# Kernel optimization log

Hardware: AMD Instinct MI355X
Metric: run time of the kernel (lower is better)

Reference implementation:

```python
import jax, jax.numpy as jnp
import numpy as np

TARGET_H, TARGET_W = 352, 352
# source spatial sizes for bottom1..bottom11 (all exact divisors of 352)
SRC_SIZES = [176, 88, 44, 22, 11, 176, 88, 44, 22, 11, 176]


def _block_resize(x, H, W):
    """Faithful jax version of simple_resize: nearest-neighbor block upsample
    with integer-floor steps, zero-filled remainder (zero here since sizes divide)."""
    h, w = x.shape[2], x.shape[3]
    xs, ys = H // h, W // w
    r = jnp.repeat(jnp.repeat(x, xs, axis=2), ys, axis=3)  # (1,1,h*xs,w*ys)
    return jnp.pad(r, ((0, 0), (0, 0), (0, H - r.shape[2]), (0, W - r.shape[3])))


def setup_inputs() -> dict:
    key = jax.random.key(0)
    keys = jax.random.split(key, 12)
    inp = {"bottom0": jax.random.normal(keys[0], (1, 1, TARGET_H, TARGET_W), dtype=jnp.float32)}
    for i, s in enumerate(SRC_SIZES, start=1):
        inp[f"bottom{i}"] = jax.random.normal(keys[i], (1, 1, s, s), dtype=jnp.float32)
    return inp


def reference(bottom0, bottom1, bottom2, bottom3, bottom4, bottom5,
              bottom6, bottom7, bottom8, bottom9, bottom10, bottom11):
    H, W = bottom0.shape[2], bottom0.shape[3]
    rest = [bottom1, bottom2, bottom3, bottom4, bottom5, bottom6,
            bottom7, bottom8, bottom9, bottom10, bottom11]
    datum = [bottom0]
    for b in rest:
        datum.append(b if b.shape == bottom0.shape else _block_resize(b, H, W))
    return jnp.concatenate(datum, axis=1)  # (1, 12, 352, 352)
```

## Files before the change

### kernel.cpp

```cpp
#include <hip/hip_runtime.h>


#define TARGET 352
#define PLANE (TARGET * TARGET)

struct Ptrs { const float* p[12]; };

__global__ __launch_bounds__(256) void resize_cat_kernel(Ptrs ptrs, float* __restrict__ out) {
    const int c = blockIdx.y;
    const int t = blockIdx.x * blockDim.x + threadIdx.x;
    const int e = t * 4;
    const int y = e / TARGET;
    const int x = e - y * TARGET;

    static const __device__ int d_shift[12] = {0, 1, 2, 3, 4, 5, 1, 2, 3, 4, 5, 1};
    static const __device__ int d_srcsz[12] = {TARGET, 176, 88, 44, 22, 11, 176, 88, 44, 22, 11, 176};

    const int sh = d_shift[c];
    const int s  = d_srcsz[c];
    const float* __restrict__ src = ptrs.p[c];

    float4 v;
    if (sh == 0) {
        v = *reinterpret_cast<const float4*>(src + e);
    } else {
        const float* row = src + (y >> sh) * s;
        if (sh >= 2) {
            const float vv = row[x >> sh];
            v = make_float4(vv, vv, vv, vv);
        } else {
            const float a = row[x >> 1];
            const float b = row[(x >> 1) + 1];
            v = make_float4(a, a, b, b);
        }
    }
    *reinterpret_cast<float4*>(out + c * PLANE + e) = v;
}

extern "C" void kernel_launch(void* const* d_in, const int* in_sizes, int n_in,
                              void* d_out, int out_size, void* d_ws, size_t ws_size,
                              hipStream_t stream) {
    Ptrs ptrs;
    for (int i = 0; i < 12; ++i) ptrs.p[i] = (const float*)d_in[i];
    float* out = (float*)d_out;

    dim3 grid(121, 12);
    resize_cat_kernel<<<grid, 256, 0, stream>>>(ptrs, out);
}
```

Baseline: 11.18 us.

## Process four channels per thread with compile-time resize parameters

Each thread now produces four output channels instead of one, and the grid shrinks from 12 to 3 channel groups. Shift and source size become template constants, so the device-memory lookup tables and runtime branching go away. The intent is more memory operations in flight per thread and less per-thread index overhead. In exchange, the grid has only 363 blocks, which may underfill the GPU's compute units and reduce the latency hiding that many blocks provide.

```diff
diff --git a/kernel.cpp b/kernel.cpp
--- a/kernel.cpp
+++ b/kernel.cpp
@@ -6,35 +6,53 @@
 
 struct Ptrs { const float* p[12]; };
 
+template <int SH, int SRCSZ>
+__device__ __forceinline__ float4 fetch(const float* __restrict__ src, int e, int y, int x) {
+    if constexpr (SH == 0) {
+        return *reinterpret_cast<const float4*>(src + e);
+    } else if constexpr (SH == 1) {
+        const float* row = src + (y >> 1) * SRCSZ;
+        const float a = row[x >> 1];
+        const float b = row[(x >> 1) + 1];
+        return make_float4(a, a, b, b);
+    } else {
+        const float* row = src + (y >> SH) * SRCSZ;
+        const float v = row[x >> SH];
+        return make_float4(v, v, v, v);
+    }
+}
+
+
 __global__ __launch_bounds__(256) void resize_cat_kernel(Ptrs ptrs, float* __restrict__ out) {
-    const int c = blockIdx.y;
+    const int g = blockIdx.y;
     const int t = blockIdx.x * blockDim.x + threadIdx.x;
     const int e = t * 4;
     const int y = e / TARGET;
     const int x = e - y * TARGET;
 
-    static const __device__ int d_shift[12] = {0, 1, 2, 3, 4, 5, 1, 2, 3, 4, 5, 1};
-    static const __device__ int d_srcsz[12] = {TARGET, 176, 88, 44, 22, 11, 176, 88, 44, 22, 11, 176};
+    float4 v0, v1, v2, v3;
+    if (g == 0) {
+        v0 = fetch<0, TARGET>(ptrs.p[0], e, y, x);
+        v1 = fetch<1, 176  >(ptrs.p[1], e, y, x);
+        v2 = fetch<2, 88   >(ptrs.p[2], e, y, x);
+        v3 = fetch<3, 44   >(ptrs.p[3], e, y, x);
+    } else if (g == 1) {
+        v0 = fetch<4, 22   >(ptrs.p[4], e, y, x);
+        v1 = fetch<5, 11   >(ptrs.p[5], e, y, x);
+        v2 = fetch<1, 176  >(ptrs.p[6], e, y, x);
+        v3 = fetch<2, 88   >(ptrs.p[7], e, y, x);
+    } else {
+        v0 = fetch<3, 44   >(ptrs.p[8], e, y, x);
+        v1 = fetch<4, 22   >(ptrs.p[9], e, y, x);
+        v2 = fetch<5, 11   >(ptrs.p[10], e, y, x);
+        v3 = fetch<1, 176  >(ptrs.p[11], e, y, x);
+    }
 
-    const int sh = d_shift[c];
-    const int s  = d_srcsz[c];
-    const float* __restrict__ src = ptrs.p[c];
-
-    float4 v;
-    if (sh == 0) {
-        v = *reinterpret_cast<const float4*>(src + e);
-    } else {
-        const float* row = src + (y >> sh) * s;
-        if (sh >= 2) {
-            const float vv = row[x >> sh];
-            v = make_float4(vv, vv, vv, vv);
-        } else {
-            const float a = row[x >> 1];
-            const float b = row[(x >> 1) + 1];
-            v = make_float4(a, a, b, b);
-        }
-    }
-    *reinterpret_cast<float4*>(out + c * PLANE + e) = v;
+    float* base = out + g * 4 * PLANE + e;
+    *reinterpret_cast<float4*>(base + 0 * PLANE) = v0;
+    *reinterpret_cast<float4*>(base + 1 * PLANE) = v1;
+    *reinterpret_cast<float4*>(base + 2 * PLANE) = v2;
+    *reinterpret_cast<float4*>(base + 3 * PLANE) = v3;
 }
 
 extern "C" void kernel_launch(void* const* d_in, const int* in_sizes, int n_in,
@@ -44,6 +62,6 @@
     for (int i = 0; i < 12; ++i) ptrs.p[i] = (const float*)d_in[i];
     float* out = (float*)d_out;
 
-    dim3 grid(121, 12);
+    dim3 grid(121, 3);
     resize_cat_kernel<<<grid, 256, 0, stream>>>(ptrs, out);
 }
```

Result: faster. 10.21 us (-8.7%).
